# Kernel optimization log

Measured on AMD Instinct MI355X. Metric: run time of the kernel, lower is better.

Reference implementation:

```python
import jax, jax.numpy as jnp
import numpy as np

H = 1024   # hidden_size
O = 1024   # output_size
A = 2      # action_dim
B = 512    # batch
T = 64     # sequence length


def setup_inputs() -> dict:
    key = jax.random.key(0)
    ks = jax.random.split(key, 6)
    s = 0.05  # init scale for stability of the recurrent loop
    return {
        "enc": jax.random.normal(ks[0], (B, O), jnp.float32),
        "actions": jax.random.normal(ks[1], (T, B, A), jnp.float32),
        "h0": jnp.zeros((1, B, H), jnp.float32),
        "W_ih": jax.random.normal(ks[2], (3 * H, A + O), jnp.float32) * s,
        "W_hh": jax.random.normal(ks[3], (3 * H, H), jnp.float32) * s,
        "b_ih": jnp.zeros((3 * H,), jnp.float32),
        "b_hh": jnp.zeros((3 * H,), jnp.float32),
        "W_out": jax.random.normal(ks[4], (O, H), jnp.float32) * s,
        "b_out": jnp.zeros((O,), jnp.float32),
    }


def _gru_cell(x, h, W_ih, W_hh, b_ih, b_hh):
    # torch GRU gate order: r, z, n
    gi = x @ W_ih.T + b_ih           # [B, 3H]
    gh = h @ W_hh.T + b_hh           # [B, 3H]
    gi_r, gi_z, gi_n = jnp.split(gi, 3, axis=1)
    gh_r, gh_z, gh_n = jnp.split(gh, 3, axis=1)
    r = jax.nn.sigmoid(gi_r + gh_r)
    z = jax.nn.sigmoid(gi_z + gh_z)
    n = jnp.tanh(gi_n + r * gh_n)
    return (1.0 - z) * n + z * h


def reference(enc, actions, h0, W_ih, W_hh, b_ih, b_hh, W_out, b_out):
    """predict_sequence: autoregressive GRU loop, output projection fed back as next enc."""
    def step(carry, a_t):
        h, e = carry                              # h: [B,H], e: [B,O]
        x = jnp.concatenate([e, a_t], axis=1)     # [B, O+A]
        h_new = _gru_cell(x, h, W_ih, W_hh, b_ih, b_hh)
        out = h_new @ W_out.T + b_out             # [B, O]
        return (h_new, out), out

    _, outputs = jax.lax.scan(step, (h0[0], enc), actions)
    return outputs  # [T, B, O]
```

## Files before the change

### kernel.cpp

```cpp
#include <hip/hip_runtime.h>
#include <stdint.h>
#include <stddef.h>


typedef _Float16 f16x8 __attribute__((ext_vector_type(8)));
typedef float f32x4  __attribute__((ext_vector_type(4)));

__device__ __forceinline__ void split2h(float v, _Float16& a, _Float16& b) {
    a = (_Float16)v;
    b = (_Float16)((v - (float)a) * 2048.0f);
}

__device__ __forceinline__ int swz(int row, int col) {
    return row * 128 + (col ^ ((row & 7) << 4));
}

__device__ __forceinline__ void gload16(const char* src, char* ldsdst) {
    __builtin_amdgcn_global_load_lds(
        (const __attribute__((address_space(1))) void*)src,
        (__attribute__((address_space(3))) void*)ldsdst, 16, 0, 0);
}

__global__ __launch_bounds__(256) void gemm_step64(
    const _Float16* __restrict__ hc0, const _Float16* __restrict__ hc1,
    const _Float16* __restrict__ W0,  const _Float16* __restrict__ W1,
    _Float16* __restrict__ hn0, _Float16* __restrict__ hn1,
    float* __restrict__ h32,
    float* __restrict__ outp,
    const float* __restrict__ bias_big,
    const float* __restrict__ W_ih,
    const float* __restrict__ act,
    int is_final)
{
    __shared__ alignas(16) char lds[32768];
    const int bid = blockIdx.x;
    int mt, nt;
    if (is_final) { mt = bid & 7; nt = 64 + (bid >> 3); }
    else { const int xcd = bid & 7, loc = bid >> 3;
           mt = loc & 7; nt = xcd * 10 + (loc >> 3); }
    const int nrow0 = (nt < 64) ? nt * 64 : 4096 + (nt - 64) * 64;

    const int tid  = threadIdx.x;
    const int wid  = tid >> 6;
    const int lane = tid & 63;
    const int wr = wid >> 1, wc = wid & 1;
    const int l16 = lane & 15, lq = lane >> 4;
    const int srcsw = (((lane & 7) ^ ((lane >> 3) & 7)) << 4);
    const int lrow = lane >> 3;

    const size_t aoff0 = (size_t)(mt * 64 + wid * 16 + lrow) * 2048 + srcsw;
    const size_t aoff1 = aoff0 + 8 * 2048;
    const size_t boff0 = (size_t)(nrow0 + wid * 16 + lrow) * 2048 + srcsw;
    const size_t boff1 = boff0 + 8 * 2048;
    const int dst0 = (wid * 16) * 128;
    const int dst1 = (wid * 16 + 8) * 128;

    f32x4 acc0[2][2] = {}, accL[2][2] = {};

    for (int kt = 0; kt < 16; ++kt) {
        const int ko = kt * 128;
        gload16((const char*)hc0 + aoff0 + ko, lds + dst0);
        gload16((const char*)hc0 + aoff1 + ko, lds + dst1);
        gload16((const char*)hc1 + aoff0 + ko, lds + 8192 + dst0);
        gload16((const char*)hc1 + aoff1 + ko, lds + 8192 + dst1);
        gload16((const char*)W0  + boff0 + ko, lds + 16384 + dst0);
        gload16((const char*)W0  + boff1 + ko, lds + 16384 + dst1);
        gload16((const char*)W1  + boff0 + ko, lds + 24576 + dst0);
        gload16((const char*)W1  + boff1 + ko, lds + 24576 + dst1);
        __syncthreads();

#pragma unroll
        for (int kk = 0; kk < 2; ++kk) {
            const int col = kk * 64 + lq * 16;
            f16x8 af0[2], af1[2], bf0[2], bf1[2];
#pragma unroll
            for (int mi = 0; mi < 2; ++mi) {
                const int ad = swz(wr * 32 + mi * 16 + l16, col);
                af0[mi] = *(const f16x8*)(lds + ad);
                af1[mi] = *(const f16x8*)(lds + 8192 + ad);
            }
#pragma unroll
            for (int ni = 0; ni < 2; ++ni) {
                const int bd = swz(wc * 32 + ni * 16 + l16, col);
                bf0[ni] = *(const f16x8*)(lds + 16384 + bd);
                bf1[ni] = *(const f16x8*)(lds + 24576 + bd);
            }
#pragma unroll
            for (int mi = 0; mi < 2; ++mi)
#pragma unroll
                for (int ni = 0; ni < 2; ++ni)
                    acc0[mi][ni] = __builtin_amdgcn_mfma_f32_16x16x32_f16(
                        af0[mi], bf0[ni], acc0[mi][ni], 0, 0, 0);
#pragma unroll
            for (int mi = 0; mi < 2; ++mi)
#pragma unroll
                for (int ni = 0; ni < 2; ++ni)
                    accL[mi][ni] = __builtin_amdgcn_mfma_f32_16x16x32_f16(
                        af0[mi], bf1[ni], accL[mi][ni], 0, 0, 0);
#pragma unroll
            for (int mi = 0; mi < 2; ++mi)
#pragma unroll
                for (int ni = 0; ni < 2; ++ni)
                    accL[mi][ni] = __builtin_amdgcn_mfma_f32_16x16x32_f16(
                        af1[mi], bf0[ni], accL[mi][ni], 0, 0, 0);
        }
        __syncthreads();
    }

    if (nt >= 64) {
#pragma unroll
        for (int ni = 0; ni < 2; ++ni) {
            const int oc = (nt - 64) * 64 + wc * 32 + ni * 16 + l16;
            const float bias = bias_big[4096 + oc];
#pragma unroll
            for (int mi = 0; mi < 2; ++mi)
#pragma unroll
                for (int r = 0; r < 4; ++r) {
                    const int brow = mt * 64 + wr * 32 + mi * 16 + lq * 4 + r;
                    const float v = (acc0[mi][ni][r]
                                   + accL[mi][ni][r] * (1.f/2048.f)) * (1.f/16.f)
                                  + bias;
                    outp[(size_t)brow * 1024 + oc] = v;
                }
        }
        return;
    }
    const int gate = lane & 3;
#pragma unroll
    for (int ni = 0; ni < 2; ++ni) {
        const int c = nt * 64 + wc * 32 + ni * 16 + l16;
        const int u = c >> 2;
        const int orig_n = gate * 1024 + u;
        const float bias = bias_big[orig_n];
        float w0 = 0.f, w1 = 0.f;
        if (gate < 3) { w0 = W_ih[(size_t)orig_n * 1026 + 1024];
                        w1 = W_ih[(size_t)orig_n * 1026 + 1025]; }
#pragma unroll
        for (int mi = 0; mi < 2; ++mi)
#pragma unroll
            for (int r = 0; r < 4; ++r) {
                const int brow = mt * 64 + wr * 32 + mi * 16 + lq * 4 + r;
                const float v = (acc0[mi][ni][r]
                               + accL[mi][ni][r] * (1.f/2048.f)) * (1.f/16.f)
                              + bias
                              + act[brow * 2] * w0 + act[brow * 2 + 1] * w1;
                const float o1 = __shfl_xor(v, 1);
                const float o2 = __shfl_xor(v, 2);
                const float o3 = __shfl_xor(v, 3);
                if (gate == 0) {
                    const float rr = 1.f / (1.f + expf(-v));
                    const float zz = 1.f / (1.f + expf(-o1));
                    const float nn = tanhf(o2 + rr * o3);
                    const size_t o = (size_t)brow * 1024 + u;
                    const float hnew = (1.f - zz) * nn + zz * h32[o];
                    h32[o] = hnew;
                    _Float16 a, b; split2h(hnew, a, b);
                    hn0[o] = a; hn1[o] = b;
                }
            }
    }
}

__device__ __forceinline__ void stage_regs(
    const _Float16* __restrict__ A0, const _Float16* __restrict__ A1,
    const _Float16* __restrict__ B0, const _Float16* __restrict__ B1,
    int mrow0, int nrow0, int wid, int lr, int lc, int kt,
    f16x8 (&ra0)[4], f16x8 (&ra1)[4], f16x8 (&rb0)[2], f16x8 (&rb1)[2])
{
    const int koff = kt * 128 + lc;
    const char* a0 = (const char*)A0 + koff;
    const char* a1 = (const char*)A1 + koff;
    const char* b0 = (const char*)B0 + koff;
    const char* b1 = (const char*)B1 + koff;
#pragma unroll
    for (int j = 0; j < 4; ++j) {
        const size_t ro = (size_t)(mrow0 + wid * 32 + j * 8 + lr) * 2048;
        ra0[j] = *(const f16x8*)(a0 + ro);
        ra1[j] = *(const f16x8*)(a1 + ro);
    }
#pragma unroll
    for (int j = 0; j < 2; ++j) {
        const size_t ro = (size_t)(nrow0 + wid * 16 + j * 8 + lr) * 2048;
        rb0[j] = *(const f16x8*)(b0 + ro);
        rb1[j] = *(const f16x8*)(b1 + ro);
    }
}

__device__ __forceinline__ void gemm_core3t(
    const _Float16* __restrict__ A0, const _Float16* __restrict__ A1,
    const _Float16* __restrict__ B0, const _Float16* __restrict__ B1,
    int mrow0, int nrow0, char* lds,
    f32x4 (&acc0)[4][2], f32x4 (&accL)[4][2])
{
    const int tid  = threadIdx.x;
    const int wid  = tid >> 6;
    const int lane = tid & 63;
    const int wr = wid >> 1, wc = wid & 1;
    const int l16 = lane & 15, lq = lane >> 4;
    const int lr = lane >> 3, lc = (lane & 7) << 4;
    const int sw = lc ^ (lr << 4);

    f16x8 pa0[4], pa1[4], pb0[2], pb1[2];
    f16x8 na0[4], na1[4], nb0[2], nb1[2];
    stage_regs(A0, A1, B0, B1, mrow0, nrow0, wid, lr, lc, 0, pa0, pa1, pb0, pb1);

    for (int kt = 0; kt < 16; ++kt) {
        if (kt < 15)
            stage_regs(A0, A1, B0, B1, mrow0, nrow0, wid, lr, lc, kt + 1,
                       na0, na1, nb0, nb1);
        __syncthreads();
#pragma unroll
        for (int j = 0; j < 4; ++j) {
            const int ro = (wid * 32 + j * 8 + lr) * 128 + sw;
            *(f16x8*)(lds + ro)         = pa0[j];
            *(f16x8*)(lds + 16384 + ro) = pa1[j];
        }
#pragma unroll
        for (int j = 0; j < 2; ++j) {
            const int ro = (wid * 16 + j * 8 + lr) * 128 + sw;
            *(f16x8*)(lds + 32768 + ro) = pb0[j];
            *(f16x8*)(lds + 40960 + ro) = pb1[j];
        }
        __syncthreads();

#pragma unroll
        for (int kk = 0; kk < 2; ++kk) {
            const int col = kk * 64 + lq * 16;
            f16x8 af0[4], af1[4], bf0[2], bf1[2];
#pragma unroll
            for (int mi = 0; mi < 4; ++mi) {
                const int ad = swz(wr * 64 + mi * 16 + l16, col);
                af0[mi] = *(const f16x8*)(lds + ad);
                af1[mi] = *(const f16x8*)(lds + 16384 + ad);
            }
#pragma unroll
            for (int ni = 0; ni < 2; ++ni) {
                const int bd = swz(wc * 32 + ni * 16 + l16, col);
                bf0[ni] = *(const f16x8*)(lds + 32768 + bd);
                bf1[ni] = *(const f16x8*)(lds + 40960 + bd);
            }
#pragma unroll
            for (int mi = 0; mi < 4; ++mi)
#pragma unroll
                for (int ni = 0; ni < 2; ++ni)
                    acc0[mi][ni] = __builtin_amdgcn_mfma_f32_16x16x32_f16(
                        af0[mi], bf0[ni], acc0[mi][ni], 0, 0, 0);
#pragma unroll
            for (int mi = 0; mi < 4; ++mi)
#pragma unroll
                for (int ni = 0; ni < 2; ++ni)
                    accL[mi][ni] = __builtin_amdgcn_mfma_f32_16x16x32_f16(
                        af0[mi], bf1[ni], accL[mi][ni], 0, 0, 0);
#pragma unroll
            for (int mi = 0; mi < 4; ++mi)
#pragma unroll
                for (int ni = 0; ni < 2; ++ni)
                    accL[mi][ni] = __builtin_amdgcn_mfma_f32_16x16x32_f16(
                        af1[mi], bf0[ni], accL[mi][ni], 0, 0, 0);
        }
        if (kt < 15) {
#pragma unroll
            for (int j = 0; j < 4; ++j) { pa0[j] = na0[j]; pa1[j] = na1[j]; }
#pragma unroll
            for (int j = 0; j < 2; ++j) { pb0[j] = nb0[j]; pb1[j] = nb1[j]; }
        }
    }
}

__global__ __launch_bounds__(256) void gemm_t0_16(
    const _Float16* __restrict__ e0, const _Float16* __restrict__ e1,
    const _Float16* __restrict__ hA0, const _Float16* __restrict__ hA1,
    const _Float16* __restrict__ Wih0, const _Float16* __restrict__ Wih1,
    const _Float16* __restrict__ Whh0, const _Float16* __restrict__ Whh1,
    const float* __restrict__ W_ih,
    const float* __restrict__ b_ih, const float* __restrict__ b_hh,
    const float* __restrict__ act,
    float* __restrict__ gbuf)
{
    __shared__ alignas(16) char lds[49152];
    const int bid = blockIdx.x;
    const int mt = bid & 3, nt = bid >> 2;
    const _Float16 *A0, *A1, *B0, *B1; int nr0;
    if (nt < 48) { A0 = e0;  A1 = e1;  B0 = Wih0; B1 = Wih1; nr0 = nt * 64; }
    else         { A0 = hA0; A1 = hA1; B0 = Whh0; B1 = Whh1; nr0 = (nt - 48) * 64; }
    f32x4 acc0[4][2] = {}, accL[4][2] = {};
    gemm_core3t(A0, A1, B0, B1, mt * 128, nr0, lds, acc0, accL);

    const int lane = threadIdx.x & 63, wid = threadIdx.x >> 6;
    const int wr = wid >> 1, wc = wid & 1, l16 = lane & 15, lq = lane >> 4;
#pragma unroll
    for (int ni = 0; ni < 2; ++ni) {
        const int ncol = nt * 64 + wc * 32 + ni * 16 + l16;
        float bias, w0 = 0.f, w1 = 0.f;
        if (ncol < 3072) {
            bias = b_ih[ncol];
            w0 = W_ih[(size_t)ncol * 1026 + 1024];
            w1 = W_ih[(size_t)ncol * 1026 + 1025];
        } else bias = b_hh[ncol - 3072];
#pragma unroll
        for (int mi = 0; mi < 4; ++mi)
#pragma unroll
            for (int r = 0; r < 4; ++r) {
                const int brow = mt * 128 + wr * 64 + mi * 16 + lq * 4 + r;
                const float v = (acc0[mi][ni][r]
                               + accL[mi][ni][r] * (1.f/2048.f)) * (1.f/16.f)
                              + bias
                              + act[brow * 2] * w0 + act[brow * 2 + 1] * w1;
                gbuf[(size_t)brow * 6144 + ncol] = v;
            }
    }
}

__global__ __launch_bounds__(256) void gemm_wcomb16(
    const _Float16* __restrict__ Wih0, const _Float16* __restrict__ Wih1,
    const _Float16* __restrict__ WoT0, const _Float16* __restrict__ WoT1,
    const float* __restrict__ W_hh,
    _Float16* __restrict__ W0, _Float16* __restrict__ W1)
{
    __shared__ alignas(16) char lds[49152];
    const int bid = blockIdx.x;
    const int mt = bid >> 4, nt = bid & 15;
    f32x4 acc0[4][2] = {}, accL[4][2] = {};
    gemm_core3t(Wih0, Wih1, WoT0, WoT1, mt * 128, nt * 64, lds, acc0, accL);

    const int lane = threadIdx.x & 63, wid = threadIdx.x >> 6;
    const int wr = wid >> 1, wc = wid & 1, l16 = lane & 15, lq = lane >> 4;
#pragma unroll
    for (int ni = 0; ni < 2; ++ni) {
        const int c = nt * 64 + wc * 32 + ni * 16 + l16;
#pragma unroll
        for (int mi = 0; mi < 4; ++mi)
#pragma unroll
            for (int r = 0; r < 4; ++r) {
                const int i = mt * 128 + wr * 64 + mi * 16 + lq * 4 + r;
                float v = (acc0[mi][ni][r]
                         + accL[mi][ni][r] * (1.f/2048.f)) * (1.f/256.f);
                if (i < 2048) v += W_hh[(size_t)i * 1024 + c];
                const size_t nr = (size_t)(4 * (i & 1023) + (i >> 10)) * 1024 + c;
                _Float16 a, b; split2h(v * 16.0f, a, b);
                W0[nr] = a; W1[nr] = b;
            }
    }
}

__global__ __launch_bounds__(256) void ew_t0_16(
    const float* __restrict__ gbuf, float* __restrict__ h32,
    _Float16* __restrict__ hA0, _Float16* __restrict__ hA1)
{
    const int idx = blockIdx.x * 256 + threadIdx.x;
    const int b = idx >> 10, j = idx & 1023;
    const float* g = gbuf + (size_t)b * 6144;
    const float pr  = g[j]        + g[3072 + j];
    const float pz  = g[1024 + j] + g[4096 + j];
    const float r = 1.f / (1.f + expf(-pr));
    const float z = 1.f / (1.f + expf(-pz));
    const float n = tanhf(g[2048 + j] + r * g[5120 + j]);
    const float h = (1.f - z) * n + z * h32[idx];
    h32[idx] = h;
    split2h(h, hA0[idx], hA1[idx]);
}

__global__ __launch_bounds__(256) void prep_w16(
    const float* __restrict__ W_ih, const float* __restrict__ W_hh,
    const float* __restrict__ W_out,
    _Float16* __restrict__ Wih0, _Float16* __restrict__ Wih1,
    _Float16* __restrict__ Whh0, _Float16* __restrict__ Whh1,
    _Float16* __restrict__ WoT0, _Float16* __restrict__ WoT1,
    _Float16* __restrict__ W0,   _Float16* __restrict__ W1)
{
    const int idx = blockIdx.x * 256 + threadIdx.x;
    const int n = idx >> 10, k = idx & 1023;
    _Float16 a, b;
    split2h(W_ih[(size_t)n * 1026 + k] * 16.0f, a, b);
    Wih0[idx] = a; Wih1[idx] = b;
    split2h(W_hh[idx] * 16.0f, a, b);
    Whh0[idx] = a; Whh1[idx] = b;
    if (n >= 2048) {
        const size_t nr = (size_t)(4 * (n - 2048) + 3) * 1024 + k;
        W0[nr] = a; W1[nr] = b;
    }
    if (n < 1024) {
        split2h(W_out[idx] * 16.0f, a, b);
        W0[(size_t)(4096 + n) * 1024 + k] = a;
        W1[(size_t)(4096 + n) * 1024 + k] = b;
        WoT0[(size_t)k * 1024 + n] = a;
        WoT1[(size_t)k * 1024 + n] = b;
    }
}

__global__ __launch_bounds__(256) void prep_m16(
    const float* __restrict__ enc, const float* __restrict__ h0,
    const float* __restrict__ W_ih,
    const float* __restrict__ b_ih, const float* __restrict__ b_hh,
    const float* __restrict__ b_out,
    _Float16* __restrict__ e0, _Float16* __restrict__ e1,
    _Float16* __restrict__ hA0, _Float16* __restrict__ hA1,
    float* __restrict__ h32, float* __restrict__ bias_big)
{
    const int idx = blockIdx.x * 256 + threadIdx.x;
    if (idx < 524288) {
        split2h(enc[idx], e0[idx], e1[idx]);
        const float hv = h0[idx];
        h32[idx] = hv;
        split2h(hv, hA0[idx], hA1[idx]);
    } else if (idx < 524288 + 5120) {
        const int nn = idx - 524288;
        float v;
        if (nn < 3072) {
            float d = 0.f;
            for (int o = 0; o < 1024; ++o) d += W_ih[(size_t)nn * 1026 + o] * b_out[o];
            v = b_ih[nn] + d + (nn < 2048 ? b_hh[nn] : 0.f);
        } else if (nn < 4096) v = b_hh[nn - 1024];
        else                  v = b_out[nn - 4096];
        bias_big[nn] = v;
    }
}

__global__ __launch_bounds__(256) void gemm_f32(
    const float* __restrict__ A, int lda,
    const float* __restrict__ Bm, int ldb,
    const float* __restrict__ bias,
    const float* __restrict__ act,
    float* __restrict__ dst, int dst_stride, int dst_coloff)
{
    __shared__ float As[16][64];
    __shared__ float Bs[16][64];
    const int t  = threadIdx.x;
    const int tx = t & 15, ty = t >> 4;
    const int row0 = blockIdx.y * 64, col0 = blockIdx.x * 64;
    const int lm = t >> 2;
    const int lk = (t & 3) * 4;
    float acc[4][4] = {};
    for (int kt = 0; kt < 64; ++kt) {
        const int kbase = kt * 16 + lk;
        const float* ap = A + (size_t)(row0 + lm) * lda + kbase;
        const float a0 = ap[0], a1 = ap[1], a2 = ap[2], a3 = ap[3];
        const float* bp = Bm + (size_t)(col0 + lm) * ldb + kbase;
        const float b0 = bp[0], b1 = bp[1], b2 = bp[2], b3 = bp[3];
        __syncthreads();
        As[lk + 0][lm] = a0;   As[lk + 1][lm] = a1;
        As[lk + 2][lm] = a2;   As[lk + 3][lm] = a3;
        Bs[lk + 0][lm] = b0;   Bs[lk + 1][lm] = b1;
        Bs[lk + 2][lm] = b2;   Bs[lk + 3][lm] = b3;
        __syncthreads();
#pragma unroll
        for (int kk = 0; kk < 16; ++kk) {
            const f32x4 a4 = *(const f32x4*)&As[kk][ty * 4];
            const f32x4 b4 = *(const f32x4*)&Bs[kk][tx * 4];
#pragma unroll
            for (int i = 0; i < 4; ++i)
#pragma unroll
                for (int j = 0; j < 4; ++j)
                    acc[i][j] += a4[i] * b4[j];
        }
    }
#pragma unroll
    for (int i = 0; i < 4; ++i) {
        const int row = row0 + ty * 4 + i;
        float a0 = 0.f, a1 = 0.f;
        if (act) { a0 = act[row * 2]; a1 = act[row * 2 + 1]; }
#pragma unroll
        for (int j = 0; j < 4; ++j) {
            const int col = col0 + tx * 4 + j;
            float v = acc[i][j] + (bias ? bias[col] : 0.f);
            if (act) v += a0 * Bm[(size_t)col * ldb + 1024]
                        + a1 * Bm[(size_t)col * ldb + 1025];
            dst[(size_t)row * dst_stride + dst_coloff + col] = v;
        }
    }
}

__global__ __launch_bounds__(256) void ew_gru32(
    const float* __restrict__ gbuf, float* __restrict__ h32)
{
    const int idx = blockIdx.x * 256 + threadIdx.x;
    const int b = idx >> 10, j = idx & 1023;
    const float* g = gbuf + (size_t)b * 6144;
    const float pr  = g[j]        + g[3072 + j];
    const float pz  = g[1024 + j] + g[4096 + j];
    const float r = 1.f / (1.f + expf(-pr));
    const float z = 1.f / (1.f + expf(-pz));
    const float n = tanhf(g[2048 + j] + r * g[5120 + j]);
    h32[idx] = (1.f - z) * n + z * h32[idx];
}

__global__ __launch_bounds__(256) void init_h(const float* __restrict__ h0,
                                              float* __restrict__ h32) {
    const int idx = blockIdx.x * 256 + threadIdx.x;
    h32[idx] = h0[idx];
}

extern "C" void kernel_launch(void* const* d_in, const int* in_sizes, int n_in,
                              void* d_out, int out_size, void* d_ws, size_t ws_size,
                              hipStream_t stream) {
    const float* enc     = (const float*)d_in[0];
    const float* actions = (const float*)d_in[1];
    const float* h0      = (const float*)d_in[2];
    const float* W_ih    = (const float*)d_in[3];
    const float* W_hh    = (const float*)d_in[4];
    const float* b_ih    = (const float*)d_in[5];
    const float* b_hh    = (const float*)d_in[6];
    const float* W_out   = (const float*)d_in[7];
    const float* b_out   = (const float*)d_in[8];
    float* out = (float*)d_out;
    char* ws = (char*)d_ws;

    float* h32  = (float*)ws;
    float* gbuf = (float*)(ws + 2097152);

    const size_t NEED = 69226496;
    if (ws_size < NEED) {
        init_h<<<2048, 256, 0, stream>>>(h0, h32);
        const float* e = enc;
        for (int t = 0; t < 64; ++t) {
            gemm_f32<<<dim3(48, 8), 256, 0, stream>>>(
                e, 1024, W_ih, 1026, b_ih, actions + (size_t)t * 1024, gbuf, 6144, 0);
            gemm_f32<<<dim3(48, 8), 256, 0, stream>>>(
                h32, 1024, W_hh, 1024, b_hh, nullptr, gbuf, 6144, 3072);
            ew_gru32<<<2048, 256, 0, stream>>>(gbuf, h32);
            float* ot = out + (size_t)t * 524288;
            gemm_f32<<<dim3(16, 8), 256, 0, stream>>>(
                h32, 1024, W_out, 1024, b_out, nullptr, ot, 1024, 0);
            e = ot;
        }
        return;
    }

    size_t off = 14680064;
    auto take = [&](size_t bytes) { char* p = ws + off; off += bytes; return p; };
    _Float16* W0   = (_Float16*)take(10485760);
    _Float16* W1   = (_Float16*)take(10485760);
    _Float16* Wih0 = (_Float16*)take(6291456);
    _Float16* Wih1 = (_Float16*)take(6291456);
    _Float16* Whh0 = (_Float16*)take(6291456);
    _Float16* Whh1 = (_Float16*)take(6291456);
    _Float16* WoT0 = (_Float16*)take(2097152);
    _Float16* WoT1 = (_Float16*)take(2097152);
    _Float16* e0   = (_Float16*)take(1048576);
    _Float16* e1   = (_Float16*)take(1048576);
    _Float16* hA0  = (_Float16*)take(1048576);
    _Float16* hA1  = (_Float16*)take(1048576);
    float* bias_big= (float*)take(20480);
    _Float16* hB0 = (_Float16*)gbuf;
    _Float16* hB1 = (_Float16*)((char*)gbuf + 1048576);

    prep_w16<<<12288, 256, 0, stream>>>(W_ih, W_hh, W_out,
        Wih0, Wih1, Whh0, Whh1, WoT0, WoT1, W0, W1);
    prep_m16<<<2068, 256, 0, stream>>>(enc, h0, W_ih, b_ih, b_hh, b_out,
        e0, e1, hA0, hA1, h32, bias_big);
    gemm_wcomb16<<<384, 256, 0, stream>>>(Wih0, Wih1, WoT0, WoT1, W_hh, W0, W1);

    gemm_t0_16<<<384, 256, 0, stream>>>(e0, e1, hA0, hA1,
        Wih0, Wih1, Whh0, Whh1, W_ih, b_ih, b_hh, actions, gbuf);
    ew_t0_16<<<2048, 256, 0, stream>>>(gbuf, h32, hA0, hA1);

    _Float16 *c0 = hA0, *c1 = hA1, *n0 = hB0, *n1 = hB1;
    for (int t = 1; t < 64; ++t) {
        gemm_step64<<<640, 256, 0, stream>>>(c0, c1, W0, W1, n0, n1, h32,
            out + (size_t)(t - 1) * 524288, bias_big, W_ih,
            actions + (size_t)t * 1024, 0);
        _Float16* s;
        s = c0; c0 = n0; n0 = s;
        s = c1; c1 = n1; n1 = s;
    }
    gemm_step64<<<128, 256, 0, stream>>>(c0, c1, W0, W1, n0, n1, h32,
        out + (size_t)63 * 524288, bias_big, W_ih, actions, 1);
}
```

Baseline: 2.010 ms.

## Double-buffer LDS tiles to overlap global loads with MFMA compute

The per-step GEMM kernel's K loop now uses two 32KB LDS buffers. It prefetches the next K tile with direct global-to-LDS loads while MFMAs run on the current one, which drops one barrier per iteration and hides load latency. The cost is doubled LDS use (64KB per block), which may lower occupancy. The single remaining barrier also relies on its implicit vmcnt wait to make the prefetched tile visible.

```diff
diff --git a/kernel.cpp b/kernel.cpp
--- a/kernel.cpp
+++ b/kernel.cpp
@@ -32,7 +32,7 @@
     const float* __restrict__ act,
     int is_final)
 {
-    __shared__ alignas(16) char lds[32768];
+    __shared__ alignas(16) char lds[65536];
     const int bid = blockIdx.x;
     int mt, nt;
     if (is_final) { mt = bid & 7; nt = 64 + (bid >> 3); }
@@ -57,17 +57,25 @@
 
     f32x4 acc0[2][2] = {}, accL[2][2] = {};
 
+    auto stage = [&](int kt, char* buf) {
+        const int ko = kt * 128;
+        gload16((const char*)hc0 + aoff0 + ko, buf + dst0);
+        gload16((const char*)hc0 + aoff1 + ko, buf + dst1);
+        gload16((const char*)hc1 + aoff0 + ko, buf + 8192 + dst0);
+        gload16((const char*)hc1 + aoff1 + ko, buf + 8192 + dst1);
+        gload16((const char*)W0  + boff0 + ko, buf + 16384 + dst0);
+        gload16((const char*)W0  + boff1 + ko, buf + 16384 + dst1);
+        gload16((const char*)W1  + boff0 + ko, buf + 24576 + dst0);
+        gload16((const char*)W1  + boff1 + ko, buf + 24576 + dst1);
+    };
+
+    stage(0, lds);
+    __syncthreads();
+    int cur = 0;
+
     for (int kt = 0; kt < 16; ++kt) {
-        const int ko = kt * 128;
-        gload16((const char*)hc0 + aoff0 + ko, lds + dst0);
-        gload16((const char*)hc0 + aoff1 + ko, lds + dst1);
-        gload16((const char*)hc1 + aoff0 + ko, lds + 8192 + dst0);
-        gload16((const char*)hc1 + aoff1 + ko, lds + 8192 + dst1);
-        gload16((const char*)W0  + boff0 + ko, lds + 16384 + dst0);
-        gload16((const char*)W0  + boff1 + ko, lds + 16384 + dst1);
-        gload16((const char*)W1  + boff0 + ko, lds + 24576 + dst0);
-        gload16((const char*)W1  + boff1 + ko, lds + 24576 + dst1);
-        __syncthreads();
+        char* buf = lds + cur * 32768;
+        if (kt < 15) stage(kt + 1, lds + (cur ^ 1) * 32768);
 
 #pragma unroll
         for (int kk = 0; kk < 2; ++kk) {
@@ -76,14 +84,14 @@
 #pragma unroll
             for (int mi = 0; mi < 2; ++mi) {
                 const int ad = swz(wr * 32 + mi * 16 + l16, col);
-                af0[mi] = *(const f16x8*)(lds + ad);
-                af1[mi] = *(const f16x8*)(lds + 8192 + ad);
+                af0[mi] = *(const f16x8*)(buf + ad);
+                af1[mi] = *(const f16x8*)(buf + 8192 + ad);
             }
 #pragma unroll
             for (int ni = 0; ni < 2; ++ni) {
                 const int bd = swz(wc * 32 + ni * 16 + l16, col);
-                bf0[ni] = *(const f16x8*)(lds + 16384 + bd);
-                bf1[ni] = *(const f16x8*)(lds + 24576 + bd);
+                bf0[ni] = *(const f16x8*)(buf + 16384 + bd);
+                bf1[ni] = *(const f16x8*)(buf + 24576 + bd);
             }
 #pragma unroll
             for (int mi = 0; mi < 2; ++mi)
@@ -104,7 +112,10 @@
                     accL[mi][ni] = __builtin_amdgcn_mfma_f32_16x16x32_f16(
                         af1[mi], bf0[ni], accL[mi][ni], 0, 0, 0);
         }
-        __syncthreads();
+        if (kt < 15) {
+            __syncthreads();
+            cur ^= 1;
+        }
     }
 
     if (nt >= 64) {
```

Measured after the change: 2.652 ms. +31.9%, slower.
